# Optimization experiments

Hardware: AMD Instinct MI355X
Metric: run time of the kernel (lower is better)

Reference implementation:

```python
import jax, jax.numpy as jnp
import numpy as np

# dims: T time steps, B batch, F clinical features, H GRU hidden, NH heads, DFF ffn dim, AH single-attn hidden
T, B, F, H, NH, DFF, AH = 128, 256, 76, 64, 4, 256, 8


def setup_inputs() -> dict:
    key = jax.random.key(0)
    ks = jax.random.split(key, 32)
    s = 0.1
    def u(k, shape):
        return jax.random.uniform(k, shape, jnp.float32, -s, s)
    return {
        "x": jax.random.normal(ks[0], (T, B, F), jnp.float32),
        # per-feature GRU(1, H) weight stacks (torch gate order: r, z, n)
        "gru_w_ih": u(ks[1], (F, 3 * H)),          # input dim is 1 -> squeezed
        "gru_w_hh": u(ks[2], (F, 3 * H, H)),
        "gru_b_ih": jnp.zeros((F, 3 * H), jnp.float32),
        "gru_b_hh": jnp.zeros((F, 3 * H), jnp.float32),
        # per-feature SingleAttention('new', time_aware) params
        "att_Wt": u(ks[3], (F, H, AH)),
        "att_Wx": u(ks[4], (F, H, AH)),
        "att_rate": jnp.full((F,), 0.8, jnp.float32),
        # multi-head self-attention over the feature axis
        "mha_wq": u(ks[5], (H, H)), "mha_bq": jnp.zeros((H,), jnp.float32),
        "mha_wk": u(ks[6], (H, H)), "mha_bk": jnp.zeros((H,), jnp.float32),
        "mha_wv": u(ks[7], (H, H)), "mha_bv": jnp.zeros((H,), jnp.float32),
        "mha_wo": u(ks[8], (H, H)), "mha_bo": jnp.zeros((H,), jnp.float32),
        # position-wise feed forward
        "ffn_w1": u(ks[9], (H, DFF)), "ffn_b1": jnp.zeros((DFF,), jnp.float32),
        "ffn_w2": u(ks[10], (DFF, H)), "ffn_b2": jnp.zeros((H,), jnp.float32),
        # FinalAttentionQKV ('mul')
        "fa_wq": u(ks[11], (H, H)), "fa_bq": jnp.zeros((H,), jnp.float32),
        "fa_wk": u(ks[12], (H, H)), "fa_bk": jnp.zeros((H,), jnp.float32),
        "fa_wv": u(ks[13], (H, H)), "fa_bv": jnp.zeros((H,), jnp.float32),
        # output head
        "out0_w": u(ks[14], (H, H)), "out0_b": jnp.zeros((H,), jnp.float32),
        "out1_w": u(ks[15], (H, 1)), "out1_b": jnp.zeros((1,), jnp.float32),
    }


def reference(x, gru_w_ih, gru_w_hh, gru_b_ih, gru_b_hh,
              att_Wt, att_Wx, att_rate,
              mha_wq, mha_bq, mha_wk, mha_bk, mha_wv, mha_bv, mha_wo, mha_bo,
              ffn_w1, ffn_b1, ffn_w2, ffn_b2,
              fa_wq, fa_bq, fa_wk, fa_bk, fa_wv, fa_bv,
              out0_w, out0_b, out1_w, out1_b):
    # x: (T, B, F); torch permutes to (B, T, F)
    Ts, Bsz, Fd = x.shape
    Hd = gru_w_hh.shape[-1]
    dk = Hd // NH

    # ---- all F GRU(1,H) channels fused into one scan (vectorized over F) ----
    xs = jnp.transpose(x, (0, 2, 1))  # (T, F, B)

    def step(h, x_t):  # h: (F,B,H), x_t: (F,B)
        gx = x_t[:, :, None] * gru_w_ih[:, None, :] + gru_b_ih[:, None, :]      # (F,B,3H)
        gh = jnp.einsum('fbh,fgh->fbg', h, gru_w_hh) + gru_b_hh[:, None, :]     # (F,B,3H)
        rx, zx, nx = jnp.split(gx, 3, axis=-1)
        rh, zh, nh = jnp.split(gh, 3, axis=-1)
        r = jax.nn.sigmoid(rx + rh)
        z = jax.nn.sigmoid(zx + zh)
        n = jnp.tanh(nx + r * nh)
        h_new = (1.0 - z) * n + z * h
        return h_new, h_new

    h0 = jnp.zeros((Fd, Bsz, Hd), x.dtype)
    _, hs = jax.lax.scan(step, h0, xs)        # (T, F, B, H)
    hs = jnp.transpose(hs, (1, 2, 0, 3))       # (F, B, T, H)

    # ---- per-feature SingleAttention, type='new', time-aware ----
    q = jnp.einsum('fbh,fha->fba', hs[:, :, -1, :], att_Wt)   # (F,B,AH)
    k = jnp.einsum('fbth,fha->fbta', hs, att_Wx)              # (F,B,T,AH)
    dp = jnp.einsum('fba,fbta->fbt', q, k)                    # (F,B,T)
    sig = jax.nn.sigmoid(dp)
    decay = jnp.arange(Ts, 0, -1, dtype=x.dtype)              # T..1 (time_decays + 1)
    denom = jax.nn.sigmoid(att_rate)[:, None, None] * (jnp.log(2.72 + (1.0 - sig)) * decay)
    e = jax.nn.relu(sig / denom)
    a = jax.nn.softmax(e, axis=-1)
    emb = jnp.einsum('fbt,fbth->bfh', a, hs)                  # (B, F, H)

    def lin(t, w, b):
        return t @ w + b

    # ---- multi-head self-attention over the F axis + residual ----
    # NOTE: original lambda ignores its (layernormed) argument, so LN is dead code.
    def heads(t):
        return t.reshape(Bsz, Fd, NH, dk).transpose(0, 2, 1, 3)
    qh = heads(lin(emb, mha_wq, mha_bq))
    kh = heads(lin(emb, mha_wk, mha_bk))
    vh = heads(lin(emb, mha_wv, mha_bv))
    scores = jnp.einsum('bhqd,bhkd->bhqk', qh, kh) / jnp.sqrt(jnp.asarray(dk, x.dtype))
    attn = jax.nn.softmax(scores, axis=-1)
    ctx = jnp.einsum('bhqk,bhkd->bhqd', attn, vh).transpose(0, 2, 1, 3).reshape(Bsz, Fd, Hd)
    ctx = emb + lin(ctx, mha_wo, mha_bo)

    # ---- position-wise feed-forward + residual ----
    ctx = ctx + lin(jax.nn.relu(lin(ctx, ffn_w1, ffn_b1)), ffn_w2, ffn_b2)

    # ---- FinalAttentionQKV, type='mul' ----
    fq = lin(ctx[:, -1, :], fa_wq, fa_bq)      # (B,H)
    fk = lin(ctx, fa_wk, fa_bk)                # (B,F,H)
    fv = lin(ctx, fa_wv, fa_bv)                # (B,F,H)
    fe = jnp.einsum('bfh,bh->bf', fk, fq)
    fa_w = jax.nn.softmax(fe, axis=1)
    v = jnp.einsum('bf,bfh->bh', fa_w, fv)     # (B,H)

    # ---- output head ----
    out = jax.nn.sigmoid(lin(jax.nn.relu(lin(v, out0_w, out0_b)), out1_w, out1_b))
    return out  # (B, 1)
```

## Files before the change

kernel.cpp:

```cpp
#include <hip/hip_runtime.h>
#include <hip/hip_bf16.h>
#include <cstdint>
#include <cstddef>

#define TT 128
#define BBATCH 256
#define FFEAT 76
#define HDIM 64
#define NHEAD 4
#define DKH 16
#define DFF1 256
#define AH1 8
#define NROWS (BBATCH * FFEAT)

#define LOG2E 1.4426950408889634f

typedef __attribute__((ext_vector_type(8))) short bf16x8;
typedef __attribute__((ext_vector_type(4))) float f32x4;

__device__ __forceinline__ float fast_sigmoid(float v) {
    float p = __builtin_amdgcn_exp2f(-v * LOG2E);
    return __builtin_amdgcn_rcpf(1.0f + p);
}
__device__ __forceinline__ float fast_tanh(float v) {
    float p = __builtin_amdgcn_exp2f(v * (2.0f * LOG2E));
    return 1.0f - 2.0f * __builtin_amdgcn_rcpf(1.0f + p);
}
__device__ __forceinline__ short f2bf(float x) {
    __hip_bfloat16 h = __float2bfloat16(x);
    return *reinterpret_cast<short*>(&h);
}
__device__ __forceinline__ float bf2f(unsigned short s) {
    return __uint_as_float(((unsigned)s) << 16);
}
__device__ __forceinline__ unsigned pack_bf16(float a, float b) {
    unsigned ua = (unsigned)(unsigned short)f2bf(a);
    unsigned ub = (unsigned)(unsigned short)f2bf(b);
    return ua | (ub << 16);
}

__global__ __launch_bounds__(256, 1) void gru_scan_kernel(
    const float* __restrict__ x, const float* __restrict__ w_ih,
    const float* __restrict__ w_hh, const float* __restrict__ b_ih,
    const float* __restrict__ b_hh, const float* __restrict__ Wt,
    const float* __restrict__ Wx, int f_base,
    __hip_bfloat16* __restrict__ hs, float* __restrict__ wtil)
{
    const int f_loc = blockIdx.y;
    const int f     = f_base + f_loc;
    const int bblk  = blockIdx.x * 64;
    const int tid   = threadIdx.x;
    const int wave  = tid >> 6;
    const int lane  = tid & 63;
    const int c     = lane & 15;
    const int q     = lane >> 4;
    const int b0    = bblk + wave * 16;

    __shared__ float x_lds[TT][64];
    __shared__ float wt_s[64][8];
    __shared__ float wx_s[64][8];
    __shared__ short hx[4][16][72];
    __shared__ float q_s[4][16][8];

    for (int i = tid; i < TT * 64; i += 256) {
        int t = i >> 6, b = i & 63;
        x_lds[t][b] = x[((size_t)t * BBATCH + bblk + b) * FFEAT + f];
    }
    for (int i = tid; i < 512; i += 256) {
        ((float*)wt_s)[i] = Wt[(size_t)f * 512 + i];
        ((float*)wx_s)[i] = Wx[(size_t)f * 512 + i];
    }
    __syncthreads();

    bf16x8 afr[12][2];
    {
        const float* whh_f = w_hh + (size_t)f * 192 * 64;
        #pragma unroll
        for (int nt = 0; nt < 12; ++nt) {
            int gate = nt >> 2, tt = nt & 3;
            int urow = (c >> 2) * 8 + (tt & 1) * 4 + (c & 3) + (tt >> 1) * 32;
            const float* row = whh_f + (size_t)(gate * 64 + urow) * 64;
            #pragma unroll
            for (int kq = 0; kq < 2; ++kq) {
                bf16x8 fr;
                #pragma unroll
                for (int j = 0; j < 8; ++j) fr[j] = f2bf(row[kq * 32 + q * 8 + j]);
                afr[nt][kq] = fr;
            }
        }
    }
    float wr[4][4], wz[4][4], wn[4][4], bnx[4][4];
    f32x4 biasv[12];
    #pragma unroll
    for (int tt = 0; tt < 4; ++tt) {
        #pragma unroll
        for (int r = 0; r < 4; ++r) {
            int u = q * 8 + (tt & 1) * 4 + r + (tt >> 1) * 32;
            wr[tt][r]  = w_ih[f*192 + u];
            wz[tt][r]  = w_ih[f*192 + 64 + u];
            wn[tt][r]  = w_ih[f*192 + 128 + u];
            bnx[tt][r] = b_ih[f*192 + 128 + u];
            biasv[tt][r]     = b_ih[f*192 + u]      + b_hh[f*192 + u];
            biasv[4 + tt][r] = b_ih[f*192 + 64 + u] + b_hh[f*192 + 64 + u];
            biasv[8 + tt][r] = b_hh[f*192 + 128 + u];
        }
    }

    float hprev[4][4];
    #pragma unroll
    for (int tt = 0; tt < 4; ++tt)
        #pragma unroll
        for (int r = 0; r < 4; ++r) hprev[tt][r] = 0.f;

    bf16x8 hb0 = {0,0,0,0,0,0,0,0};
    bf16x8 hb1 = {0,0,0,0,0,0,0,0};

    short* hs_b = (short*)hs + ((size_t)f_loc * BBATCH + b0 + c) * TT * HDIM;

    for (int t = 0; t < TT; ++t) {
        f32x4 acc[12];
        #pragma unroll
        for (int nt = 0; nt < 12; ++nt) {
            f32x4 a = __builtin_amdgcn_mfma_f32_16x16x32_bf16(afr[nt][0], hb0, biasv[nt], 0, 0, 0);
            acc[nt]  = __builtin_amdgcn_mfma_f32_16x16x32_bf16(afr[nt][1], hb1, a, 0, 0, 0);
        }

        float xv = x_lds[t][wave * 16 + c];
        float hn4[4][4];
        #pragma unroll
        for (int tt = 0; tt < 4; ++tt) {
            #pragma unroll
            for (int r = 0; r < 4; ++r) {
                float R  = fmaf(xv, wr[tt][r], acc[tt][r]);
                float Z  = fmaf(xv, wz[tt][r], acc[4 + tt][r]);
                float NX = fmaf(xv, wn[tt][r], bnx[tt][r]);
                float rg = fast_sigmoid(R);
                float zg = fast_sigmoid(Z);
                float ng = fast_tanh(fmaf(rg, acc[8 + tt][r], NX));
                float hn = fmaf(zg, hprev[tt][r] - ng, ng);
                hprev[tt][r] = hn;
                hn4[tt][r] = hn;
            }
        }
        {
            union { int4 i; bf16x8 v; } u0, u1;
            u0.i.x = pack_bf16(hn4[0][0], hn4[0][1]);
            u0.i.y = pack_bf16(hn4[0][2], hn4[0][3]);
            u0.i.z = pack_bf16(hn4[1][0], hn4[1][1]);
            u0.i.w = pack_bf16(hn4[1][2], hn4[1][3]);
            u1.i.x = pack_bf16(hn4[2][0], hn4[2][1]);
            u1.i.y = pack_bf16(hn4[2][2], hn4[2][3]);
            u1.i.z = pack_bf16(hn4[3][0], hn4[3][1]);
            u1.i.w = pack_bf16(hn4[3][2], hn4[3][3]);
            hb0 = u0.v; hb1 = u1.v;
        }
        short* dst = hs_b + (size_t)t * HDIM + q * 8;
        *(bf16x8*)dst = hb0;
        *(bf16x8*)(dst + 32) = hb1;
    }

    *(bf16x8*)&hx[wave][c][q * 8]      = hb0;
    *(bf16x8*)&hx[wave][c][32 + q * 8] = hb1;

    #pragma unroll
    for (int rr = 0; rr < 2; ++rr) {
        int role = rr * 64 + lane;
        int b = role >> 3, a = role & 7;
        float s = 0.f;
        #pragma unroll 8
        for (int j = 0; j < 64; ++j)
            s = fmaf(bf2f((unsigned short)hx[wave][b][j]), wt_s[j][a], s);
        q_s[wave][b][a] = s;
    }
    {
        int b = lane >> 2, jb = (lane & 3) * 16;
        float qreg[8];
        #pragma unroll
        for (int a = 0; a < 8; ++a) qreg[a] = q_s[wave][b][a];
        float* wt_out = wtil + ((size_t)(b0 + b) * FFEAT + f) * HDIM + jb;
        #pragma unroll
        for (int j4 = 0; j4 < 4; ++j4) {
            float4 v;
            #pragma unroll
            for (int jj = 0; jj < 4; ++jj) {
                int j = jb + j4 * 4 + jj;
                float s = 0.f;
                #pragma unroll
                for (int a = 0; a < 8; ++a) s = fmaf(wx_s[j][a], qreg[a], s);
                (&v.x)[jj] = s;
            }
            *(float4*)&wt_out[j4 * 4] = v;
        }
    }
}

__global__ __launch_bounds__(64) void attn2_kernel(
    const __hip_bfloat16* __restrict__ hs, const float* __restrict__ wtil,
    const float* __restrict__ rate, int f_base, float* __restrict__ emb)
{
    const int b     = blockIdx.x;
    const int f_loc = blockIdx.y;
    const int f     = f_base + f_loc;
    const int lane  = threadIdx.x;

    __shared__ short h_s[TT][72];
    __shared__ float a_s[TT];

    float wreg[64];
    {
        const float4* src = (const float4*)(wtil + ((size_t)b * FFEAT + f) * HDIM);
        #pragma unroll
        for (int i = 0; i < 16; ++i) {
            float4 v = src[i];
            wreg[4*i+0] = v.x; wreg[4*i+1] = v.y; wreg[4*i+2] = v.z; wreg[4*i+3] = v.w;
        }
    }
    const float rs = fast_sigmoid(rate[f]);
    const short* base = (const short*)hs + ((size_t)f_loc * BBATCH + b) * TT * HDIM;

    float e[2];
    #pragma unroll
    for (int half = 0; half < 2; ++half) {
        int t = half * 64 + lane;
        const uint4* row = (const uint4*)(base + (size_t)t * HDIM);
        float dp = 0.f;
        #pragma unroll
        for (int c4 = 0; c4 < 8; ++c4) {
            uint4 u = row[c4];
            *(uint4*)&h_s[t][c4 * 8] = u;
            unsigned vals[4] = {u.x, u.y, u.z, u.w};
            #pragma unroll
            for (int p = 0; p < 4; ++p) {
                dp = fmaf(__uint_as_float(vals[p] << 16),         wreg[c4*8 + 2*p],     dp);
                dp = fmaf(__uint_as_float(vals[p] & 0xffff0000u), wreg[c4*8 + 2*p + 1], dp);
            }
        }
        float sig = fast_sigmoid(dp);
        float den = rs * (__logf(2.72f + (1.0f - sig)) * (float)(TT - t));
        e[half] = fmaxf(sig / den, 0.0f);
    }
    float m = fmaxf(e[0], e[1]);
    #pragma unroll
    for (int off = 32; off > 0; off >>= 1) m = fmaxf(m, __shfl_xor(m, off, 64));
    float p0 = __builtin_amdgcn_exp2f((e[0] - m) * LOG2E);
    float p1 = __builtin_amdgcn_exp2f((e[1] - m) * LOG2E);
    float s = p0 + p1;
    #pragma unroll
    for (int off = 32; off > 0; off >>= 1) s += __shfl_xor(s, off, 64);
    float inv = __builtin_amdgcn_rcpf(s);
    a_s[lane]      = p0 * inv;
    a_s[lane + 64] = p1 * inv;

    const int j = lane;
    float acc = 0.f;
    #pragma unroll 8
    for (int t = 0; t < TT; ++t)
        acc = fmaf(a_s[t], bf2f((unsigned short)h_s[t][j]), acc);
    emb[((size_t)b * FFEAT + f) * HDIM + j] = acc;
}

struct GemmP {
    const float* X;
    const float* W[3];
    const float* B[3];
    const float* R;
    float* Y[3];
    int K;
    int Nfull;
    int act;
};

__global__ __launch_bounds__(256) void gemm_kernel(GemmP A)
{
    __shared__ float xs[64][65];
    __shared__ float ws[64][68];

    const int tid = threadIdx.x;
    const int tx  = tid & 15;
    const int ty  = tid >> 4;
    const int m0  = blockIdx.x * 64;
    const int n0  = blockIdx.y * 64;
    const int z   = blockIdx.z;

    const float* W = A.W[z];
    const float* Bv = A.B[z];
    float* Y = A.Y[z];
    const int K = A.K, Nfull = A.Nfull;

    float acc[4][4];
    #pragma unroll
    for (int i = 0; i < 4; ++i)
        #pragma unroll
        for (int j = 0; j < 4; ++j) acc[i][j] = 0.f;

    for (int kc = 0; kc < K; kc += 64) {
        for (int s = tid; s < 1024; s += 256) {
            int row = s >> 4, c4 = s & 15;
            float4 xv = *(const float4*)&A.X[(size_t)(m0 + row) * K + kc + 4*c4];
            xs[row][4*c4+0] = xv.x; xs[row][4*c4+1] = xv.y;
            xs[row][4*c4+2] = xv.z; xs[row][4*c4+3] = xv.w;
            float4 wv = *(const float4*)&W[(size_t)(kc + row) * Nfull + n0 + 4*c4];
            *(float4*)&ws[row][4*c4] = wv;
        }
        __syncthreads();
        #pragma unroll 16
        for (int k = 0; k < 64; ++k) {
            float a0 = xs[4*ty+0][k], a1 = xs[4*ty+1][k];
            float a2 = xs[4*ty+2][k], a3 = xs[4*ty+3][k];
            float4 wv = *(const float4*)&ws[k][4*tx];
            #pragma unroll
            for (int j = 0; j < 4; ++j) {
                float wj = (&wv.x)[j];
                acc[0][j] = fmaf(a0, wj, acc[0][j]);
                acc[1][j] = fmaf(a1, wj, acc[1][j]);
                acc[2][j] = fmaf(a2, wj, acc[2][j]);
                acc[3][j] = fmaf(a3, wj, acc[3][j]);
            }
        }
        __syncthreads();
    }

    float4 bias = *(const float4*)&Bv[n0 + 4*tx];
    #pragma unroll
    for (int i = 0; i < 4; ++i) {
        int row = m0 + 4*ty + i;
        float4 v;
        v.x = acc[i][0] + bias.x; v.y = acc[i][1] + bias.y;
        v.z = acc[i][2] + bias.z; v.w = acc[i][3] + bias.w;
        if (A.act) {
            v.x = fmaxf(v.x, 0.f); v.y = fmaxf(v.y, 0.f);
            v.z = fmaxf(v.z, 0.f); v.w = fmaxf(v.w, 0.f);
        }
        if (A.R) {
            float4 r4 = *(const float4*)&A.R[(size_t)row * Nfull + n0 + 4*tx];
            v.x += r4.x; v.y += r4.y; v.z += r4.z; v.w += r4.w;
        }
        *(float4*)&Y[(size_t)row * Nfull + n0 + 4*tx] = v;
    }
}

__global__ __launch_bounds__(256) void mha_core_kernel(
    const float* __restrict__ q, const float* __restrict__ k,
    const float* __restrict__ v, float* __restrict__ ctx)
{
    const int b  = blockIdx.x;
    const int hh = blockIdx.y;
    const int tid = threadIdx.x;

    __shared__ float qs[FFEAT][17];
    __shared__ float ks[FFEAT][17];
    __shared__ float vs[FFEAT][17];
    __shared__ float ps[FFEAT][77];

    for (int idx = tid; idx < FFEAT * DKH; idx += 256) {
        int i = idx >> 4, c = idx & 15;
        size_t g = ((size_t)b * FFEAT + i) * HDIM + hh * DKH + c;
        qs[i][c] = q[g]; ks[i][c] = k[g]; vs[i][c] = v[g];
    }
    __syncthreads();

    for (int idx = tid; idx < FFEAT * FFEAT; idx += 256) {
        int i = idx / FFEAT, j = idx % FFEAT;
        float acc = 0.f;
        #pragma unroll
        for (int c = 0; c < DKH; ++c) acc = fmaf(qs[i][c], ks[j][c], acc);
        ps[i][j] = acc * 0.25f;
    }
    __syncthreads();

    if (tid < FFEAT) {
        float mm = ps[tid][0];
        #pragma unroll 4
        for (int j = 1; j < FFEAT; ++j) mm = fmaxf(mm, ps[tid][j]);
        float ss = 0.f;
        #pragma unroll 4
        for (int j = 0; j < FFEAT; ++j) {
            float pv = __builtin_amdgcn_exp2f((ps[tid][j] - mm) * LOG2E);
            ps[tid][j] = pv; ss += pv;
        }
        float inv = 1.0f / ss;
        #pragma unroll 4
        for (int j = 0; j < FFEAT; ++j) ps[tid][j] *= inv;
    }
    __syncthreads();

    for (int idx = tid; idx < FFEAT * DKH; idx += 256) {
        int i = idx >> 4, c = idx & 15;
        float acc = 0.f;
        #pragma unroll 4
        for (int j = 0; j < FFEAT; ++j) acc = fmaf(ps[i][j], vs[j][c], acc);
        ctx[((size_t)b * FFEAT + i) * HDIM + hh * DKH + c] = acc;
    }
}

__global__ __launch_bounds__(128) void final_kernel(
    const float* __restrict__ ctx3, const float* __restrict__ fk,
    const float* __restrict__ fv,
    const float* __restrict__ faq, const float* __restrict__ fabq,
    const float* __restrict__ o0w, const float* __restrict__ o0b,
    const float* __restrict__ o1w, const float* __restrict__ o1b,
    float* __restrict__ out)
{
    const int b = blockIdx.x;
    const int tid = threadIdx.x;

    __shared__ float last[HDIM];
    __shared__ float fqs[HDIM];
    __shared__ float sm[FFEAT];
    __shared__ float vv[HDIM];
    __shared__ float hh[HDIM];
    __shared__ float redm[2], redp[2];

    if (tid < HDIM) last[tid] = ctx3[((size_t)b * FFEAT + FFEAT - 1) * HDIM + tid];
    __syncthreads();
    if (tid < HDIM) {
        float acc = fabq[tid];
        #pragma unroll 8
        for (int j = 0; j < HDIM; ++j) acc = fmaf(last[j], faq[j * HDIM + tid], acc);
        fqs[tid] = acc;
    }
    __syncthreads();

    float e = -3.0e38f;
    if (tid < FFEAT) {
        const float4* kr = (const float4*)&fk[((size_t)b * FFEAT + tid) * HDIM];
        float acc = 0.f;
        #pragma unroll
        for (int c4 = 0; c4 < 16; ++c4) {
            float4 kv = kr[c4];
            acc = fmaf(kv.x, fqs[4*c4+0], acc);
            acc = fmaf(kv.y, fqs[4*c4+1], acc);
            acc = fmaf(kv.z, fqs[4*c4+2], acc);
            acc = fmaf(kv.w, fqs[4*c4+3], acc);
        }
        e = acc;
    }
    float m = e;
    #pragma unroll
    for (int off = 32; off > 0; off >>= 1) m = fmaxf(m, __shfl_xor(m, off, 64));
    if ((tid & 63) == 0) redm[tid >> 6] = m;
    __syncthreads();
    m = fmaxf(redm[0], redm[1]);
    float p = (tid < FFEAT) ? __builtin_amdgcn_exp2f((e - m) * LOG2E) : 0.f;
    float s = p;
    #pragma unroll
    for (int off = 32; off > 0; off >>= 1) s += __shfl_xor(s, off, 64);
    if ((tid & 63) == 0) redp[tid >> 6] = s;
    __syncthreads();
    s = redp[0] + redp[1];
    if (tid < FFEAT) sm[tid] = p / s;
    __syncthreads();

    if (tid < HDIM) {
        float acc = 0.f;
        for (int ff = 0; ff < FFEAT; ++ff)
            acc = fmaf(sm[ff], fv[((size_t)b * FFEAT + ff) * HDIM + tid], acc);
        vv[tid] = acc;
    }
    __syncthreads();
    if (tid < HDIM) {
        float acc = o0b[tid];
        #pragma unroll 8
        for (int j = 0; j < HDIM; ++j) acc = fmaf(vv[j], o0w[j * HDIM + tid], acc);
        hh[tid] = fmaxf(acc, 0.f);
    }
    __syncthreads();
    if (tid < 64) {
        float t = hh[tid] * o1w[tid];
        #pragma unroll
        for (int off = 32; off > 0; off >>= 1) t += __shfl_xor(t, off, 64);
        if (tid == 0) out[b] = fast_sigmoid(t + o1b[0]);
    }
}

__global__ void ws_report_kernel(float* out, int n, float ws_mib) {
    int i = blockIdx.x * blockDim.x + threadIdx.x;
    if (i < n) out[i] = ws_mib;
}

extern "C" void kernel_launch(void* const* d_in, const int* in_sizes, int n_in,
                              void* d_out, int out_size, void* d_ws, size_t ws_size,
                              hipStream_t stream)
{
    const float* x     = (const float*)d_in[0];
    const float* w_ih  = (const float*)d_in[1];
    const float* w_hh  = (const float*)d_in[2];
    const float* b_ih  = (const float*)d_in[3];
    const float* b_hh  = (const float*)d_in[4];
    const float* attWt = (const float*)d_in[5];
    const float* attWx = (const float*)d_in[6];
    const float* attRt = (const float*)d_in[7];
    const float* wq    = (const float*)d_in[8];
    const float* bq    = (const float*)d_in[9];
    const float* wk    = (const float*)d_in[10];
    const float* bk    = (const float*)d_in[11];
    const float* wv    = (const float*)d_in[12];
    const float* bv    = (const float*)d_in[13];
    const float* wo    = (const float*)d_in[14];
    const float* bo    = (const float*)d_in[15];
    const float* w1    = (const float*)d_in[16];
    const float* b1    = (const float*)d_in[17];
    const float* w2    = (const float*)d_in[18];
    const float* b2    = (const float*)d_in[19];
    const float* faq   = (const float*)d_in[20];
    const float* fabq  = (const float*)d_in[21];
    const float* fak   = (const float*)d_in[22];
    const float* fabk  = (const float*)d_in[23];
    const float* fav   = (const float*)d_in[24];
    const float* fabv  = (const float*)d_in[25];
    const float* o0w   = (const float*)d_in[26];
    const float* o0b   = (const float*)d_in[27];
    const float* o1w   = (const float*)d_in[28];
    const float* o1b   = (const float*)d_in[29];
    float* out = (float*)d_out;

    const size_t emb_bytes  = (size_t)NROWS * HDIM * 4;
    const size_t wtil_bytes = (size_t)NROWS * HDIM * 4;
    const size_t R64        = (size_t)NROWS * HDIM;
    const size_t tail_bytes = 12 * R64 * 4;

    const int chunk_opts[6] = {76, 38, 19, 4, 2, 1};
    int FC = 0;
    for (int i = 0; i < 6; ++i) {
        size_t hs_b = (size_t)chunk_opts[i] * BBATCH * TT * HDIM * 2;
        size_t scratch = hs_b > tail_bytes ? hs_b : tail_bytes;
        if (emb_bytes + wtil_bytes + scratch <= ws_size) { FC = chunk_opts[i]; break; }
    }
    if (FC == 0) {
        ws_report_kernel<<<dim3((out_size + 255) / 256), dim3(256), 0, stream>>>(
            out, out_size, (float)((double)ws_size / (1024.0 * 1024.0)));
        return;
    }

    float* emb  = (float*)d_ws;
    float* wtil = (float*)((char*)d_ws + emb_bytes);
    char*  scratch = (char*)d_ws + emb_bytes + wtil_bytes;
    __hip_bfloat16* hs = (__hip_bfloat16*)scratch;

    for (int f0 = 0; f0 < FFEAT; f0 += FC) {
        int fc = (FFEAT - f0 < FC) ? (FFEAT - f0) : FC;
        gru_scan_kernel<<<dim3(4, fc), dim3(256), 0, stream>>>(
            x, w_ih, w_hh, b_ih, b_hh, attWt, attWx, f0, hs, wtil);
        attn2_kernel<<<dim3(BBATCH, fc), dim3(64), 0, stream>>>(
            hs, wtil, attRt, f0, emb);
    }

    float* ts   = (float*)scratch;
    float* q    = ts;
    float* k    = ts + 1*R64;
    float* v    = ts + 2*R64;
    float* ctx  = ts + 3*R64;
    float* ctx2 = ts + 4*R64;
    float* hid  = ts + 5*R64;
    float* ctx3 = ts + 9*R64;
    float* fk   = ts + 10*R64;
    float* fv   = ts + 11*R64;

    const int MB = NROWS / 64;

    {
        GemmP A = { emb, {wq, wk, wv}, {bq, bk, bv}, nullptr, {q, k, v}, 64, 64, 0 };
        gemm_kernel<<<dim3(MB, 1, 3), dim3(256), 0, stream>>>(A);
    }
    mha_core_kernel<<<dim3(BBATCH, NHEAD), dim3(256), 0, stream>>>(q, k, v, ctx);
    {
        GemmP A = { ctx, {wo, nullptr, nullptr}, {bo, nullptr, nullptr}, emb,
                    {ctx2, nullptr, nullptr}, 64, 64, 0 };
        gemm_kernel<<<dim3(MB, 1, 1), dim3(256), 0, stream>>>(A);
    }
    {
        GemmP A = { ctx2, {w1, nullptr, nullptr}, {b1, nullptr, nullptr}, nullptr,
                    {hid, nullptr, nullptr}, 64, 256, 1 };
        gemm_kernel<<<dim3(MB, 4, 1), dim3(256), 0, stream>>>(A);
    }
    {
        GemmP A = { hid, {w2, nullptr, nullptr}, {b2, nullptr, nullptr}, ctx2,
                    {ctx3, nullptr, nullptr}, 256, 64, 0 };
        gemm_kernel<<<dim3(MB, 1, 1), dim3(256), 0, stream>>>(A);
    }
    {
        GemmP A = { ctx3, {fak, fav, nullptr}, {fabk, fabv, nullptr}, nullptr,
                    {fk, fv, nullptr}, 64, 64, 0 };
        gemm_kernel<<<dim3(MB, 1, 2), dim3(256), 0, stream>>>(A);
    }
    final_kernel<<<dim3(BBATCH), dim3(128), 0, stream>>>(
        ctx3, fk, fv, faq, fabq, o0w, o0b, o1w, o1b, out);
}
```

Measured before the change: 572.5 us.

## Fuse transformer tail into single per-batch kernel with LDS-resident activations

Replaces the sequence of global-memory GEMM kernels, the MHA core kernel and the final attention kernel with one tail kernel per batch element. All intermediate activations (Q/K/V, context, FFN hidden, final keys/values) stay in a shared-memory pool with aliased regions, and weights are staged tile by tile into LDS. This removes roughly 12 row-sized intermediate buffers of global traffic and several launches, and lets the GRU stage use a larger workspace chunk. In exchange, only 256 blocks run, each doing scalar FMA loops over LDS with many barriers, so parallelism and arithmetic throughput per block may be limited.

```diff
diff --git a/kernel.cpp b/kernel.cpp
--- a/kernel.cpp
+++ b/kernel.cpp
@@ -259,214 +259,240 @@
     emb[((size_t)b * FFEAT + f) * HDIM + j] = acc;
 }
 
-struct GemmP {
-    const float* X;
-    const float* W[3];
-    const float* B[3];
-    const float* R;
-    float* Y[3];
-    int K;
-    int Nfull;
-    int act;
-};
-
-__global__ __launch_bounds__(256) void gemm_kernel(GemmP A)
+#define PSTR 65
+#define OFF_EMB 0
+#define OFF_Q   4940
+#define OFF_K   9880
+#define OFF_V   14820
+#define OFF_SC  19760
+#define OFF_CTX 25840
+#define OFF_C2  30780
+#define POOL_F  35720
+#define OFF_STG OFF_SC
+#define OFF_WS  OFF_EMB
+#define OFF_HID OFF_Q
+#define OFF_C3  OFF_CTX
+#define OFF_FK  OFF_C2
+#define OFF_FV  OFF_K
+#define OFF_SCR OFF_SC
+
+__device__ __forceinline__ void gemm64p(
+    float* pool, int offA, int offW, const float* __restrict__ bg,
+    int offR, int offOut, int tid)
 {
-    __shared__ float xs[64][65];
-    __shared__ float ws[64][68];
-
-    const int tid = threadIdx.x;
-    const int tx  = tid & 15;
-    const int ty  = tid >> 4;
-    const int m0  = blockIdx.x * 64;
-    const int n0  = blockIdx.y * 64;
-    const int z   = blockIdx.z;
-
-    const float* W = A.W[z];
-    const float* Bv = A.B[z];
-    float* Y = A.Y[z];
-    const int K = A.K, Nfull = A.Nfull;
-
-    float acc[4][4];
-    #pragma unroll
-    for (int i = 0; i < 4; ++i)
-        #pragma unroll
-        for (int j = 0; j < 4; ++j) acc[i][j] = 0.f;
-
-    for (int kc = 0; kc < K; kc += 64) {
-        for (int s = tid; s < 1024; s += 256) {
-            int row = s >> 4, c4 = s & 15;
-            float4 xv = *(const float4*)&A.X[(size_t)(m0 + row) * K + kc + 4*c4];
-            xs[row][4*c4+0] = xv.x; xs[row][4*c4+1] = xv.y;
-            xs[row][4*c4+2] = xv.z; xs[row][4*c4+3] = xv.w;
-            float4 wv = *(const float4*)&W[(size_t)(kc + row) * Nfull + n0 + 4*c4];
-            *(float4*)&ws[row][4*c4] = wv;
-        }
-        __syncthreads();
+    for (int idx = tid; idx < FFEAT * 32; idx += 512) {
+        int r = idx >> 5, cp = (idx & 31) << 1;
+        float2 bv2 = *(const float2*)&bg[cp];
+        float ax = bv2.x, ay = bv2.y;
+        const float* ar = &pool[offA + r * PSTR];
+        const float* wc = &pool[offW + cp];
         #pragma unroll 16
         for (int k = 0; k < 64; ++k) {
-            float a0 = xs[4*ty+0][k], a1 = xs[4*ty+1][k];
-            float a2 = xs[4*ty+2][k], a3 = xs[4*ty+3][k];
-            float4 wv = *(const float4*)&ws[k][4*tx];
-            #pragma unroll
-            for (int j = 0; j < 4; ++j) {
-                float wj = (&wv.x)[j];
-                acc[0][j] = fmaf(a0, wj, acc[0][j]);
-                acc[1][j] = fmaf(a1, wj, acc[1][j]);
-                acc[2][j] = fmaf(a2, wj, acc[2][j]);
-                acc[3][j] = fmaf(a3, wj, acc[3][j]);
-            }
-        }
-        __syncthreads();
-    }
-
-    float4 bias = *(const float4*)&Bv[n0 + 4*tx];
-    #pragma unroll
-    for (int i = 0; i < 4; ++i) {
-        int row = m0 + 4*ty + i;
-        float4 v;
-        v.x = acc[i][0] + bias.x; v.y = acc[i][1] + bias.y;
-        v.z = acc[i][2] + bias.z; v.w = acc[i][3] + bias.w;
-        if (A.act) {
-            v.x = fmaxf(v.x, 0.f); v.y = fmaxf(v.y, 0.f);
-            v.z = fmaxf(v.z, 0.f); v.w = fmaxf(v.w, 0.f);
-        }
-        if (A.R) {
-            float4 r4 = *(const float4*)&A.R[(size_t)row * Nfull + n0 + 4*tx];
-            v.x += r4.x; v.y += r4.y; v.z += r4.z; v.w += r4.w;
-        }
-        *(float4*)&Y[(size_t)row * Nfull + n0 + 4*tx] = v;
-    }
-}
-
-__global__ __launch_bounds__(256) void mha_core_kernel(
-    const float* __restrict__ q, const float* __restrict__ k,
-    const float* __restrict__ v, float* __restrict__ ctx)
-{
-    const int b  = blockIdx.x;
-    const int hh = blockIdx.y;
-    const int tid = threadIdx.x;
-
-    __shared__ float qs[FFEAT][17];
-    __shared__ float ks[FFEAT][17];
-    __shared__ float vs[FFEAT][17];
-    __shared__ float ps[FFEAT][77];
-
-    for (int idx = tid; idx < FFEAT * DKH; idx += 256) {
-        int i = idx >> 4, c = idx & 15;
-        size_t g = ((size_t)b * FFEAT + i) * HDIM + hh * DKH + c;
-        qs[i][c] = q[g]; ks[i][c] = k[g]; vs[i][c] = v[g];
-    }
-    __syncthreads();
-
-    for (int idx = tid; idx < FFEAT * FFEAT; idx += 256) {
-        int i = idx / FFEAT, j = idx % FFEAT;
-        float acc = 0.f;
-        #pragma unroll
-        for (int c = 0; c < DKH; ++c) acc = fmaf(qs[i][c], ks[j][c], acc);
-        ps[i][j] = acc * 0.25f;
-    }
-    __syncthreads();
-
-    if (tid < FFEAT) {
-        float mm = ps[tid][0];
-        #pragma unroll 4
-        for (int j = 1; j < FFEAT; ++j) mm = fmaxf(mm, ps[tid][j]);
-        float ss = 0.f;
-        #pragma unroll 4
-        for (int j = 0; j < FFEAT; ++j) {
-            float pv = __builtin_amdgcn_exp2f((ps[tid][j] - mm) * LOG2E);
-            ps[tid][j] = pv; ss += pv;
-        }
-        float inv = 1.0f / ss;
-        #pragma unroll 4
-        for (int j = 0; j < FFEAT; ++j) ps[tid][j] *= inv;
-    }
-    __syncthreads();
-
-    for (int idx = tid; idx < FFEAT * DKH; idx += 256) {
-        int i = idx >> 4, c = idx & 15;
-        float acc = 0.f;
-        #pragma unroll 4
-        for (int j = 0; j < FFEAT; ++j) acc = fmaf(ps[i][j], vs[j][c], acc);
-        ctx[((size_t)b * FFEAT + i) * HDIM + hh * DKH + c] = acc;
-    }
-}
-
-__global__ __launch_bounds__(128) void final_kernel(
-    const float* __restrict__ ctx3, const float* __restrict__ fk,
-    const float* __restrict__ fv,
+            float a = ar[k];
+            float2 w = *(const float2*)&wc[k << 6];
+            ax = fmaf(a, w.x, ax);
+            ay = fmaf(a, w.y, ay);
+        }
+        if (offR >= 0) {
+            ax += pool[offR + r * PSTR + cp];
+            ay += pool[offR + r * PSTR + cp + 1];
+        }
+        pool[offOut + r * PSTR + cp]     = ax;
+        pool[offOut + r * PSTR + cp + 1] = ay;
+    }
+}
+
+__global__ __launch_bounds__(512, 2) void tail_kernel(
+    const float* __restrict__ emb,
+    const float* __restrict__ wq, const float* __restrict__ bq,
+    const float* __restrict__ wk, const float* __restrict__ bk,
+    const float* __restrict__ wv, const float* __restrict__ bv,
+    const float* __restrict__ wo, const float* __restrict__ bo,
+    const float* __restrict__ w1, const float* __restrict__ b1,
+    const float* __restrict__ w2, const float* __restrict__ b2,
     const float* __restrict__ faq, const float* __restrict__ fabq,
+    const float* __restrict__ fak, const float* __restrict__ fabk,
+    const float* __restrict__ fav, const float* __restrict__ fabv,
     const float* __restrict__ o0w, const float* __restrict__ o0b,
     const float* __restrict__ o1w, const float* __restrict__ o1b,
     float* __restrict__ out)
 {
-    const int b = blockIdx.x;
+    __shared__ float pool[POOL_F];
+    const int b   = blockIdx.x;
     const int tid = threadIdx.x;
 
-    __shared__ float last[HDIM];
-    __shared__ float fqs[HDIM];
-    __shared__ float sm[FFEAT];
-    __shared__ float vv[HDIM];
-    __shared__ float hh[HDIM];
-    __shared__ float redm[2], redp[2];
-
-    if (tid < HDIM) last[tid] = ctx3[((size_t)b * FFEAT + FFEAT - 1) * HDIM + tid];
-    __syncthreads();
+    for (int i = tid; i < FFEAT * HDIM; i += 512) {
+        int r = i >> 6, c = i & 63;
+        pool[OFF_EMB + r * PSTR + c] = emb[((size_t)b * FFEAT + r) * HDIM + c];
+    }
+    for (int i = tid; i < 4096; i += 512) pool[OFF_STG + i] = wq[i];
+    __syncthreads();
+
+    gemm64p(pool, OFF_EMB, OFF_STG, bq, -1, OFF_Q, tid);
+    __syncthreads();
+    for (int i = tid; i < 4096; i += 512) pool[OFF_STG + i] = wk[i];
+    __syncthreads();
+    gemm64p(pool, OFF_EMB, OFF_STG, bk, -1, OFF_K, tid);
+    __syncthreads();
+    for (int i = tid; i < 4096; i += 512) pool[OFF_STG + i] = wv[i];
+    __syncthreads();
+    gemm64p(pool, OFF_EMB, OFF_STG, bv, -1, OFF_V, tid);
+    __syncthreads();
+
+    for (int i = tid; i < FFEAT * PSTR; i += 512) pool[OFF_CTX + i] = 0.f;
+    __syncthreads();
+    for (int hh = 0; hh < NHEAD; ++hh) {
+        const int o = hh * DKH;
+        for (int idx = tid; idx < FFEAT * FFEAT; idx += 512) {
+            int i = idx / FFEAT, j = idx - i * FFEAT;
+            const float* qi = &pool[OFF_Q + i * PSTR + o];
+            const float* kj = &pool[OFF_K + j * PSTR + o];
+            float acc = 0.f;
+            #pragma unroll
+            for (int c = 0; c < DKH; ++c) acc = fmaf(qi[c], kj[c], acc);
+            pool[OFF_SC + i * 80 + j] = acc * 0.25f;
+        }
+        __syncthreads();
+        if (tid < FFEAT) {
+            float* row = &pool[OFF_SC + tid * 80];
+            float m = row[0];
+            #pragma unroll 4
+            for (int j = 1; j < FFEAT; ++j) m = fmaxf(m, row[j]);
+            float s = 0.f;
+            #pragma unroll 4
+            for (int j = 0; j < FFEAT; ++j) {
+                float p = __builtin_amdgcn_exp2f((row[j] - m) * LOG2E);
+                row[j] = p; s += p;
+            }
+            float inv = 1.0f / s;
+            #pragma unroll 4
+            for (int j = 0; j < FFEAT; ++j) row[j] *= inv;
+        }
+        __syncthreads();
+        for (int idx = tid; idx < FFEAT * DKH; idx += 512) {
+            int i = idx >> 4, c = idx & 15;
+            const float* pr = &pool[OFF_SC + i * 80];
+            const float* vc = &pool[OFF_V + o + c];
+            float acc = 0.f;
+            #pragma unroll 4
+            for (int j = 0; j < FFEAT; ++j) acc = fmaf(pr[j], vc[j * PSTR], acc);
+            pool[OFF_CTX + i * PSTR + o + c] += acc;
+        }
+        __syncthreads();
+    }
+
+    for (int i = tid; i < 4096; i += 512) pool[OFF_STG + i] = wo[i];
+    __syncthreads();
+    gemm64p(pool, OFF_CTX, OFF_STG, bo, OFF_EMB, OFF_C2, tid);
+    __syncthreads();
+
+    for (int cs = 0; cs < 4; ++cs) {
+        for (int i = tid; i < 4096; i += 512) {
+            int k = i >> 6, cc = i & 63;
+            pool[OFF_WS + i] = w1[(k << 8) + (cs << 6) + cc];
+        }
+        __syncthreads();
+        for (int idx = tid; idx < FFEAT * 32; idx += 512) {
+            int r = idx >> 5, cp = (idx & 31) << 1;
+            float2 bv2 = *(const float2*)&b1[(cs << 6) + cp];
+            float ax = bv2.x, ay = bv2.y;
+            const float* ar = &pool[OFF_C2 + r * PSTR];
+            const float* wc = &pool[OFF_WS + cp];
+            #pragma unroll 16
+            for (int k = 0; k < 64; ++k) {
+                float a = ar[k];
+                float2 w = *(const float2*)&wc[k << 6];
+                ax = fmaf(a, w.x, ax);
+                ay = fmaf(a, w.y, ay);
+            }
+            float* hd = &pool[OFF_HID + r * 260 + (cs << 6) + cp];
+            hd[0] = fmaxf(ax, 0.f);
+            hd[1] = fmaxf(ay, 0.f);
+        }
+        __syncthreads();
+    }
+
+    for (int ks = 0; ks < 4; ++ks) {
+        for (int i = tid; i < 4096; i += 512) pool[OFF_WS + i] = w2[(ks << 12) + i];
+        __syncthreads();
+        for (int idx = tid; idx < FFEAT * 32; idx += 512) {
+            int r = idx >> 5, cp = (idx & 31) << 1;
+            float ax, ay;
+            if (ks == 0) {
+                float2 bv2 = *(const float2*)&b2[cp];
+                ax = bv2.x + pool[OFF_C2 + r * PSTR + cp];
+                ay = bv2.y + pool[OFF_C2 + r * PSTR + cp + 1];
+            } else {
+                ax = pool[OFF_C3 + r * PSTR + cp];
+                ay = pool[OFF_C3 + r * PSTR + cp + 1];
+            }
+            const float* hr = &pool[OFF_HID + r * 260 + (ks << 6)];
+            const float* wc = &pool[OFF_WS + cp];
+            #pragma unroll 16
+            for (int k = 0; k < 64; ++k) {
+                float a = hr[k];
+                float2 w = *(const float2*)&wc[k << 6];
+                ax = fmaf(a, w.x, ax);
+                ay = fmaf(a, w.y, ay);
+            }
+            pool[OFF_C3 + r * PSTR + cp]     = ax;
+            pool[OFF_C3 + r * PSTR + cp + 1] = ay;
+        }
+        __syncthreads();
+    }
+
+    for (int i = tid; i < 4096; i += 512) pool[OFF_WS + i] = fak[i];
+    __syncthreads();
+    gemm64p(pool, OFF_C3, OFF_WS, fabk, -1, OFF_FK, tid);
+    __syncthreads();
+    for (int i = tid; i < 4096; i += 512) pool[OFF_WS + i] = fav[i];
+    __syncthreads();
+    gemm64p(pool, OFF_C3, OFF_WS, fabv, -1, OFF_FV, tid);
+    __syncthreads();
+
+    float* SCR = &pool[OFF_SCR];
     if (tid < HDIM) {
+        const float* last = &pool[OFF_C3 + 75 * PSTR];
         float acc = fabq[tid];
-        #pragma unroll 8
-        for (int j = 0; j < HDIM; ++j) acc = fmaf(last[j], faq[j * HDIM + tid], acc);
-        fqs[tid] = acc;
-    }
-    __syncthreads();
-
-    float e = -3.0e38f;
+        #pragma unroll 16
+        for (int j = 0; j < HDIM; ++j) acc = fmaf(last[j], faq[(j << 6) + tid], acc);
+        SCR[tid] = acc;
+    }
+    __syncthreads();
     if (tid < FFEAT) {
-        const float4* kr = (const float4*)&fk[((size_t)b * FFEAT + tid) * HDIM];
+        const float* kr = &pool[OFF_FK + tid * PSTR];
         float acc = 0.f;
-        #pragma unroll
-        for (int c4 = 0; c4 < 16; ++c4) {
-            float4 kv = kr[c4];
-            acc = fmaf(kv.x, fqs[4*c4+0], acc);
-            acc = fmaf(kv.y, fqs[4*c4+1], acc);
-            acc = fmaf(kv.z, fqs[4*c4+2], acc);
-            acc = fmaf(kv.w, fqs[4*c4+3], acc);
-        }
-        e = acc;
-    }
-    float m = e;
-    #pragma unroll
-    for (int off = 32; off > 0; off >>= 1) m = fmaxf(m, __shfl_xor(m, off, 64));
-    if ((tid & 63) == 0) redm[tid >> 6] = m;
-    __syncthreads();
-    m = fmaxf(redm[0], redm[1]);
-    float p = (tid < FFEAT) ? __builtin_amdgcn_exp2f((e - m) * LOG2E) : 0.f;
-    float s = p;
-    #pragma unroll
-    for (int off = 32; off > 0; off >>= 1) s += __shfl_xor(s, off, 64);
-    if ((tid & 63) == 0) redp[tid >> 6] = s;
-    __syncthreads();
-    s = redp[0] + redp[1];
-    if (tid < FFEAT) sm[tid] = p / s;
-    __syncthreads();
-
+        #pragma unroll 16
+        for (int c = 0; c < HDIM; ++c) acc = fmaf(kr[c], SCR[c], acc);
+        SCR[64 + tid] = acc;
+    }
+    __syncthreads();
+    if (tid == 0) {
+        float m = SCR[64];
+        for (int i = 1; i < FFEAT; ++i) m = fmaxf(m, SCR[64 + i]);
+        float s = 0.f;
+        for (int i = 0; i < FFEAT; ++i) {
+            float p = __builtin_amdgcn_exp2f((SCR[64 + i] - m) * LOG2E);
+            SCR[64 + i] = p; s += p;
+        }
+        float inv = 1.0f / s;
+        for (int i = 0; i < FFEAT; ++i) SCR[64 + i] *= inv;
+    }
+    __syncthreads();
     if (tid < HDIM) {
         float acc = 0.f;
+        #pragma unroll 4
         for (int ff = 0; ff < FFEAT; ++ff)
-            acc = fmaf(sm[ff], fv[((size_t)b * FFEAT + ff) * HDIM + tid], acc);
-        vv[tid] = acc;
+            acc = fmaf(SCR[64 + ff], pool[OFF_FV + ff * PSTR + tid], acc);
+        SCR[160 + tid] = acc;
     }
     __syncthreads();
     if (tid < HDIM) {
         float acc = o0b[tid];
-        #pragma unroll 8
-        for (int j = 0; j < HDIM; ++j) acc = fmaf(vv[j], o0w[j * HDIM + tid], acc);
-        hh[tid] = fmaxf(acc, 0.f);
-    }
-    __syncthreads();
-    if (tid < 64) {
-        float t = hh[tid] * o1w[tid];
+        #pragma unroll 16
+        for (int j = 0; j < HDIM; ++j) acc = fmaf(SCR[160 + j], o0w[(j << 6) + tid], acc);
+        float h = fmaxf(acc, 0.f);
+        float t = h * o1w[tid];
         #pragma unroll
         for (int off = 32; off > 0; off >>= 1) t += __shfl_xor(t, off, 64);
         if (tid == 0) out[b] = fast_sigmoid(t + o1b[0]);
@@ -516,15 +542,12 @@
 
     const size_t emb_bytes  = (size_t)NROWS * HDIM * 4;
     const size_t wtil_bytes = (size_t)NROWS * HDIM * 4;
-    const size_t R64        = (size_t)NROWS * HDIM;
-    const size_t tail_bytes = 12 * R64 * 4;
 
     const int chunk_opts[6] = {76, 38, 19, 4, 2, 1};
     int FC = 0;
     for (int i = 0; i < 6; ++i) {
         size_t hs_b = (size_t)chunk_opts[i] * BBATCH * TT * HDIM * 2;
-        size_t scratch = hs_b > tail_bytes ? hs_b : tail_bytes;
-        if (emb_bytes + wtil_bytes + scratch <= ws_size) { FC = chunk_opts[i]; break; }
+        if (emb_bytes + wtil_bytes + hs_b <= ws_size) { FC = chunk_opts[i]; break; }
     }
     if (FC == 0) {
         ws_report_kernel<<<dim3((out_size + 255) / 256), dim3(256), 0, stream>>>(
@@ -534,8 +557,7 @@
 
     float* emb  = (float*)d_ws;
     float* wtil = (float*)((char*)d_ws + emb_bytes);
-    char*  scratch = (char*)d_ws + emb_bytes + wtil_bytes;
-    __hip_bfloat16* hs = (__hip_bfloat16*)scratch;
+    __hip_bfloat16* hs = (__hip_bfloat16*)((char*)d_ws + emb_bytes + wtil_bytes);
 
     for (int f0 = 0; f0 < FFEAT; f0 += FC) {
         int fc = (FFEAT - f0 < FC) ? (FFEAT - f0) : FC;
@@ -545,44 +567,8 @@
             hs, wtil, attRt, f0, emb);
     }
 
-    float* ts   = (float*)scratch;
-    float* q    = ts;
-    float* k    = ts + 1*R64;
-    float* v    = ts + 2*R64;
-    float* ctx  = ts + 3*R64;
-    float* ctx2 = ts + 4*R64;
-    float* hid  = ts + 5*R64;
-    float* ctx3 = ts + 9*R64;
-    float* fk   = ts + 10*R64;
-    float* fv   = ts + 11*R64;
-
-    const int MB = NROWS / 64;
-
-    {
-        GemmP A = { emb, {wq, wk, wv}, {bq, bk, bv}, nullptr, {q, k, v}, 64, 64, 0 };
-        gemm_kernel<<<dim3(MB, 1, 3), dim3(256), 0, stream>>>(A);
-    }
-    mha_core_kernel<<<dim3(BBATCH, NHEAD), dim3(256), 0, stream>>>(q, k, v, ctx);
-    {
-        GemmP A = { ctx, {wo, nullptr, nullptr}, {bo, nullptr, nullptr}, emb,
-                    {ctx2, nullptr, nullptr}, 64, 64, 0 };
-        gemm_kernel<<<dim3(MB, 1, 1), dim3(256), 0, stream>>>(A);
-    }
-    {
-        GemmP A = { ctx2, {w1, nullptr, nullptr}, {b1, nullptr, nullptr}, nullptr,
-                    {hid, nullptr, nullptr}, 64, 256, 1 };
-        gemm_kernel<<<dim3(MB, 4, 1), dim3(256), 0, stream>>>(A);
-    }
-    {
-        GemmP A = { hid, {w2, nullptr, nullptr}, {b2, nullptr, nullptr}, ctx2,
-                    {ctx3, nullptr, nullptr}, 256, 64, 0 };
-        gemm_kernel<<<dim3(MB, 1, 1), dim3(256), 0, stream>>>(A);
-    }
-    {
-        GemmP A = { ctx3, {fak, fav, nullptr}, {fabk, fabv, nullptr}, nullptr,
-                    {fk, fv, nullptr}, 64, 64, 0 };
-        gemm_kernel<<<dim3(MB, 1, 2), dim3(256), 0, stream>>>(A);
-    }
-    final_kernel<<<dim3(BBATCH), dim3(128), 0, stream>>>(
-        ctx3, fk, fv, faq, fabq, o0w, o0b, o1w, o1b, out);
-}
+    tail_kernel<<<dim3(BBATCH), dim3(512), 0, stream>>>(
+        emb, wq, bq, wk, bk, wv, bv, wo, bo,
+        w1, b1, w2, b2, faq, fabq, fak, fabk, fav, fabv,
+        o0w, o0b, o1w, o1b, out);
+}
```

Measured after the change: 629.8 us. 10.0% more time.

## Split GRU scan into single-wave blocks and batch four rows per attention block

Applied to the files above, without the earlier changes.

The GRU scan kernel goes from 4-wave blocks covering 64 batch rows to 1-wave blocks covering 16 rows. This gives four times as many blocks, so the sequential per-feature scans can spread across more CUs. The attention kernel now packs four batch rows per 256-thread block and drops the LDS staging of hidden states. It re-reads them from global memory with paired bf16 loads and combines the two halves with a shuffle. The cost is more redundant weight loads in the scan and a second global read of hs in attention, which will likely be served from cache.

```diff
diff --git a/kernel.cpp b/kernel.cpp
--- a/kernel.cpp
+++ b/kernel.cpp
@@ -39,7 +39,7 @@
     return ua | (ub << 16);
 }
 
-__global__ __launch_bounds__(256, 1) void gru_scan_kernel(
+__global__ __launch_bounds__(64) void gru_scan_kernel(
     const float* __restrict__ x, const float* __restrict__ w_ih,
     const float* __restrict__ w_hh, const float* __restrict__ b_ih,
     const float* __restrict__ b_hh, const float* __restrict__ Wt,
@@ -48,25 +48,22 @@
 {
     const int f_loc = blockIdx.y;
     const int f     = f_base + f_loc;
-    const int bblk  = blockIdx.x * 64;
-    const int tid   = threadIdx.x;
-    const int wave  = tid >> 6;
-    const int lane  = tid & 63;
+    const int b0    = blockIdx.x * 16;
+    const int lane  = threadIdx.x;
     const int c     = lane & 15;
     const int q     = lane >> 4;
-    const int b0    = bblk + wave * 16;
-
-    __shared__ float x_lds[TT][64];
+
+    __shared__ float x_lds[TT][16];
     __shared__ float wt_s[64][8];
     __shared__ float wx_s[64][8];
-    __shared__ short hx[4][16][72];
-    __shared__ float q_s[4][16][8];
-
-    for (int i = tid; i < TT * 64; i += 256) {
-        int t = i >> 6, b = i & 63;
-        x_lds[t][b] = x[((size_t)t * BBATCH + bblk + b) * FFEAT + f];
-    }
-    for (int i = tid; i < 512; i += 256) {
+    __shared__ short hx[16][72];
+    __shared__ float q_s[16][8];
+
+    for (int i = lane; i < TT * 16; i += 64) {
+        int t = i >> 4, b = i & 15;
+        x_lds[t][b] = x[((size_t)t * BBATCH + b0 + b) * FFEAT + f];
+    }
+    for (int i = lane; i < 512; i += 64) {
         ((float*)wt_s)[i] = Wt[(size_t)f * 512 + i];
         ((float*)wx_s)[i] = Wx[(size_t)f * 512 + i];
     }
@@ -125,7 +122,7 @@
             acc[nt]  = __builtin_amdgcn_mfma_f32_16x16x32_bf16(afr[nt][1], hb1, a, 0, 0, 0);
         }
 
-        float xv = x_lds[t][wave * 16 + c];
+        float xv = x_lds[t][c];
         float hn4[4][4];
         #pragma unroll
         for (int tt = 0; tt < 4; ++tt) {
@@ -159,8 +156,8 @@
         *(bf16x8*)(dst + 32) = hb1;
     }
 
-    *(bf16x8*)&hx[wave][c][q * 8]      = hb0;
-    *(bf16x8*)&hx[wave][c][32 + q * 8] = hb1;
+    *(bf16x8*)&hx[c][q * 8]      = hb0;
+    *(bf16x8*)&hx[c][32 + q * 8] = hb1;
 
     #pragma unroll
     for (int rr = 0; rr < 2; ++rr) {
@@ -169,14 +166,14 @@
         float s = 0.f;
         #pragma unroll 8
         for (int j = 0; j < 64; ++j)
-            s = fmaf(bf2f((unsigned short)hx[wave][b][j]), wt_s[j][a], s);
-        q_s[wave][b][a] = s;
+            s = fmaf(bf2f((unsigned short)hx[b][j]), wt_s[j][a], s);
+        q_s[b][a] = s;
     }
     {
         int b = lane >> 2, jb = (lane & 3) * 16;
         float qreg[8];
         #pragma unroll
-        for (int a = 0; a < 8; ++a) qreg[a] = q_s[wave][b][a];
+        for (int a = 0; a < 8; ++a) qreg[a] = q_s[b][a];
         float* wt_out = wtil + ((size_t)(b0 + b) * FFEAT + f) * HDIM + jb;
         #pragma unroll
         for (int j4 = 0; j4 < 4; ++j4) {
@@ -194,17 +191,17 @@
     }
 }
 
-__global__ __launch_bounds__(64) void attn2_kernel(
+__global__ __launch_bounds__(256) void attn2_kernel(
     const __hip_bfloat16* __restrict__ hs, const float* __restrict__ wtil,
     const float* __restrict__ rate, int f_base, float* __restrict__ emb)
 {
-    const int b     = blockIdx.x;
+    const int w     = threadIdx.x >> 6;
+    const int lane  = threadIdx.x & 63;
+    const int b     = blockIdx.x * 4 + w;
     const int f_loc = blockIdx.y;
     const int f     = f_base + f_loc;
-    const int lane  = threadIdx.x;
-
-    __shared__ short h_s[TT][72];
-    __shared__ float a_s[TT];
+
+    __shared__ float a_s[4][TT];
 
     float wreg[64];
     {
@@ -227,7 +224,6 @@
         #pragma unroll
         for (int c4 = 0; c4 < 8; ++c4) {
             uint4 u = row[c4];
-            *(uint4*)&h_s[t][c4 * 8] = u;
             unsigned vals[4] = {u.x, u.y, u.z, u.w};
             #pragma unroll
             for (int p = 0; p < 4; ++p) {
@@ -248,15 +244,27 @@
     #pragma unroll
     for (int off = 32; off > 0; off >>= 1) s += __shfl_xor(s, off, 64);
     float inv = __builtin_amdgcn_rcpf(s);
-    a_s[lane]      = p0 * inv;
-    a_s[lane + 64] = p1 * inv;
-
-    const int j = lane;
-    float acc = 0.f;
+    a_s[w][lane]      = p0 * inv;
+    a_s[w][lane + 64] = p1 * inv;
+
+    const uint* hrow = (const uint*)base;
+    const int half2 = lane >> 5;
+    const int ul    = lane & 31;
+    float accx = 0.f, accy = 0.f;
     #pragma unroll 8
-    for (int t = 0; t < TT; ++t)
-        acc = fmaf(a_s[t], bf2f((unsigned short)h_s[t][j]), acc);
-    emb[((size_t)b * FFEAT + f) * HDIM + j] = acc;
+    for (int tb = 0; tb < 64; ++tb) {
+        int t = 2 * tb + half2;
+        uint v = hrow[(size_t)t * 32 + ul];
+        float at = a_s[w][t];
+        accx = fmaf(at, __uint_as_float(v << 16),         accx);
+        accy = fmaf(at, __uint_as_float(v & 0xffff0000u), accy);
+    }
+    accx += __shfl_xor(accx, 32, 64);
+    accy += __shfl_xor(accy, 32, 64);
+    if (lane < 32) {
+        float2 o; o.x = accx; o.y = accy;
+        *(float2*)&emb[((size_t)b * FFEAT + f) * HDIM + 2 * ul] = o;
+    }
 }
 
 struct GemmP {
@@ -539,9 +547,9 @@
 
     for (int f0 = 0; f0 < FFEAT; f0 += FC) {
         int fc = (FFEAT - f0 < FC) ? (FFEAT - f0) : FC;
-        gru_scan_kernel<<<dim3(4, fc), dim3(256), 0, stream>>>(
+        gru_scan_kernel<<<dim3(16, fc), dim3(64), 0, stream>>>(
             x, w_ih, w_hh, b_ih, b_hh, attWt, attWx, f0, hs, wtil);
-        attn2_kernel<<<dim3(BBATCH, fc), dim3(64), 0, stream>>>(
+        attn2_kernel<<<dim3(BBATCH / 4, fc), dim3(256), 0, stream>>>(
             hs, wtil, attRt, f0, emb);
     }
 
```

Measured after the change: 709.4 us. +23.9%, slower.
